# Optimization experiments

Hardware: AMD Instinct MI355X
Metric: run time of the kernel (lower is better)

The kernel has to match this reference:

```python
import jax, jax.numpy as jnp
import numpy as np

EPS = 1e-8  # torch CosineSimilarity default eps


def setup_inputs() -> dict:
    key = jax.random.key(0)
    k_emb, k_ei, k_w1, k_w2, k_b1, k_b2 = jax.random.split(key, 6)
    N, H, E = 50000, 256, 300000
    emb = jax.random.normal(k_emb, (N, H), dtype=jnp.float32)
    edge_index = jax.random.randint(k_ei, (2, E), 0, N, dtype=jnp.int64)
    # Xavier-uniform init for the two Linear layers (fan_in = fan_out = H)
    limit = float(np.sqrt(6.0 / (H + H)))
    W1 = jax.random.uniform(k_w1, (H, H), minval=-limit, maxval=limit, dtype=jnp.float32)
    W2 = jax.random.uniform(k_w2, (H, H), minval=-limit, maxval=limit, dtype=jnp.float32)
    b1 = jnp.zeros((H,), dtype=jnp.float32)
    b2 = jnp.zeros((H,), dtype=jnp.float32)
    return {"emb": emb, "edge_index": edge_index, "W1": W1, "b1": b1, "W2": W2, "b2": b2}


def _mlp(x, W1, b1, W2, b2):
    # Linear -> Dropout(eval: identity) -> ReLU -> Linear
    h = jax.nn.relu(x @ W1.T + b1)
    return h @ W2.T + b2


def _cosine(a, b):
    # torch.nn.CosineSimilarity(dim=1): dot / (max(||a||, eps) * max(||b||, eps))
    dot = jnp.sum(a * b, axis=1)
    na = jnp.maximum(jnp.linalg.norm(a, axis=1), EPS)
    nb = jnp.maximum(jnp.linalg.norm(b, axis=1), EPS)
    return dot / (na * nb)


def reference(emb, edge_index, W1, b1, W2, b2):
    col, row = edge_index[0], edge_index[1]
    f1 = emb[col]  # [E, H]
    f2 = emb[row]  # [E, H]
    g1 = _mlp(f1, W1, b1, W2, b2)
    g2 = _mlp(f2, W1, b1, W2, b2)
    return _cosine(g1, g2)  # [E] per-edge attention logits
```

## Files before the change

kernel.cpp:

```cpp
#include <hip/hip_runtime.h>
#include <stdint.h>

#define H 256
#define EPS 1e-8f

typedef __bf16 bf16x8 __attribute__((ext_vector_type(8)));
typedef float  f32x4  __attribute__((ext_vector_type(4)));

__device__ __forceinline__ unsigned short f2bf(float f) {
  unsigned u = __builtin_bit_cast(unsigned, f);
  u += 0x7FFFu + ((u >> 16) & 1u);
  return (unsigned short)(u >> 16);
}
__device__ __forceinline__ float bflo(unsigned u){ return __builtin_bit_cast(float, u << 16); }
__device__ __forceinline__ float bfhi(unsigned u){ return __builtin_bit_cast(float, u & 0xFFFF0000u); }

__device__ __forceinline__ void g2l16(const void* g, void* l) {
  __builtin_amdgcn_global_load_lds((__attribute__((address_space(1))) void*)g,
                                   (__attribute__((address_space(3))) void*)l, 16, 0, 0);
}

__global__ __launch_bounds__(256) void conv_bf16_kernel(
    const float* __restrict__ src, unsigned short* __restrict__ dst, int valid, int total) {
  int i = (blockIdx.x * 256 + threadIdx.x) * 4;
  if (i >= total) return;
  float4 v = make_float4(0.f, 0.f, 0.f, 0.f);
  if (i < valid) v = *(const float4*)(src + i);
  ushort4 o;
  o.x = f2bf(v.x); o.y = f2bf(v.y); o.z = f2bf(v.z); o.w = f2bf(v.w);
  *(ushort4*)(dst + i) = o;
}

template<bool RELU>
__global__ __launch_bounds__(256) void gemm_bt_kernel(
    const unsigned short* __restrict__ A,
    const unsigned short* __restrict__ B,
    const float* __restrict__ bias,
    unsigned short* __restrict__ C) {
  __shared__ unsigned short sA[128 * 32];
  __shared__ unsigned short sB[128 * 32];
  const int tid  = threadIdx.x;
  const int wave = tid >> 6, lane = tid & 63;
  const int quad = lane >> 4, l16 = lane & 15;
  const int wm = wave & 1, wn = wave >> 1;
  const size_t bm = blockIdx.x, bn = blockIdx.y;

  const int srow0 = (wave * 2 + 0) * 16 + (lane >> 2);
  const int srow1 = (wave * 2 + 1) * 16 + (lane >> 2);
  const int kch   = (lane & 3) * 8;
  const unsigned short* gA0 = A + ((bm * 128 + srow0) * H + kch);
  const unsigned short* gA1 = A + ((bm * 128 + srow1) * H + kch);
  const unsigned short* gB0 = B + ((bn * 128 + srow0) * H + kch);
  const unsigned short* gB1 = B + ((bn * 128 + srow1) * H + kch);
  unsigned short* lA0 = sA + (wave * 2 + 0) * 512 + lane * 8;
  unsigned short* lA1 = sA + (wave * 2 + 1) * 512 + lane * 8;
  unsigned short* lB0 = sB + (wave * 2 + 0) * 512 + lane * 8;
  unsigned short* lB1 = sB + (wave * 2 + 1) * 512 + lane * 8;

  f32x4 acc[4][4];
#pragma unroll
  for (int i = 0; i < 4; i++)
#pragma unroll
    for (int j = 0; j < 4; j++) acc[i][j] = (f32x4){0.f, 0.f, 0.f, 0.f};

#pragma unroll
  for (int kk = 0; kk < H / 32; ++kk) {
    const int k0 = kk * 32;
    if (kk) __syncthreads();
    g2l16(gA0 + k0, lA0);
    g2l16(gA1 + k0, lA1);
    g2l16(gB0 + k0, lB0);
    g2l16(gB1 + k0, lB1);
    __syncthreads();

    bf16x8 af[4], bfr[4];
#pragma unroll
    for (int i = 0; i < 4; i++)
      af[i] = *(const bf16x8*)(sA + ((wm * 64 + i * 16 + l16) * 32 + quad * 8));
#pragma unroll
    for (int j = 0; j < 4; j++)
      bfr[j] = *(const bf16x8*)(sB + ((wn * 64 + j * 16 + l16) * 32 + quad * 8));
#pragma unroll
    for (int i = 0; i < 4; i++)
#pragma unroll
      for (int j = 0; j < 4; j++)
        acc[i][j] = __builtin_amdgcn_mfma_f32_16x16x32_bf16(af[i], bfr[j], acc[i][j], 0, 0, 0);
  }

  const int row_base = (int)bm * 128 + wm * 64;
  const int col_base = (int)bn * 128 + wn * 64;
#pragma unroll
  for (int j = 0; j < 4; j++) {
    const int col = col_base + j * 16 + l16;
    const float bv = bias[col];
#pragma unroll
    for (int i = 0; i < 4; i++) {
#pragma unroll
      for (int r = 0; r < 4; r++) {
        const int row = row_base + i * 16 + quad * 4 + r;
        float v = acc[i][j][r] + bv;
        if (RELU) v = fmaxf(v, 0.f);
        C[(size_t)row * H + col] = f2bf(v);
      }
    }
  }
}

__global__ __launch_bounds__(256) void rownorm_kernel(
    const unsigned short* __restrict__ g, float* __restrict__ rn, int n) {
  int row = blockIdx.x * 4 + (threadIdx.x >> 6);
  if (row >= n) return;
  int lane = threadIdx.x & 63;
  uint2 a = ((const uint2*)(g + (size_t)row * H))[lane];
  float x0 = bflo(a.x), x1 = bfhi(a.x), x2 = bflo(a.y), x3 = bfhi(a.y);
  float ss = x0 * x0 + x1 * x1 + x2 * x2 + x3 * x3;
#pragma unroll
  for (int off = 32; off; off >>= 1) ss += __shfl_down(ss, off, 64);
  if (lane == 0) rn[row] = 1.f / fmaxf(sqrtf(ss), EPS);
}

__device__ __forceinline__ float dot_u4(uint4 a, uint4 b) {
  float s;
  s  = bflo(a.x) * bflo(b.x) + bfhi(a.x) * bfhi(b.x);
  s += bflo(a.y) * bflo(b.y) + bfhi(a.y) * bfhi(b.y);
  s += bflo(a.z) * bflo(b.z) + bfhi(a.z) * bfhi(b.z);
  s += bflo(a.w) * bflo(b.w) + bfhi(a.w) * bfhi(b.w);
  return s;
}

__global__ __launch_bounds__(256) void edge_cos_kernel(
    const int* __restrict__ ei, const unsigned short* __restrict__ g,
    const float* __restrict__ rn, float* __restrict__ out, int E) {
  const int lane = threadIdx.x & 63;
  const int wid  = threadIdx.x >> 6;
  const int l8   = lane & 7;
  const int sub  = lane >> 3;
  const int e    = blockIdx.x * 32 + wid * 8 + sub;
  if (e >= E) return;
  const int c = ei[e], r = ei[E + e];
  const uint4* gc = (const uint4*)(g + (size_t)c * H);
  const uint4* gr = (const uint4*)(g + (size_t)r * H);
  uint4 a0 = gc[l8], a1 = gc[l8 + 8], a2 = gc[l8 + 16], a3 = gc[l8 + 24];
  uint4 b0 = gr[l8], b1 = gr[l8 + 8], b2 = gr[l8 + 16], b3 = gr[l8 + 24];
  float d = dot_u4(a0, b0) + dot_u4(a1, b1) + dot_u4(a2, b2) + dot_u4(a3, b3);
  d += __shfl_xor(d, 4, 8);
  d += __shfl_xor(d, 2, 8);
  d += __shfl_xor(d, 1, 8);
  if (l8 == 0) out[e] = d * rn[c] * rn[r];
}

extern "C" void kernel_launch(void* const* d_in, const int* in_sizes, int n_in,
                              void* d_out, int out_size, void* d_ws, size_t ws_size,
                              hipStream_t stream) {
  const float* emb = (const float*)d_in[0];
  const int*   ei  = (const int*)d_in[1];
  const float* W1  = (const float*)d_in[2];
  const float* b1  = (const float*)d_in[3];
  const float* W2  = (const float*)d_in[4];
  const float* b2  = (const float*)d_in[5];
  float* out = (float*)d_out;

  const int NH = in_sizes[0];
  const int N  = NH / H;
  const int E  = in_sizes[1] / 2;
  const int Mp = ((N + 127) / 128) * 128;

  char* ws = (char*)d_ws;
  unsigned short* embB = (unsigned short*)ws; ws += (size_t)Mp * H * 2;
  unsigned short* hB   = (unsigned short*)ws; ws += (size_t)Mp * H * 2;
  unsigned short* gB   = (unsigned short*)ws; ws += (size_t)Mp * H * 2;
  unsigned short* w1B  = (unsigned short*)ws; ws += (size_t)H * H * 2;
  unsigned short* w2B  = (unsigned short*)ws; ws += (size_t)H * H * 2;
  float* rn            = (float*)ws;

  conv_bf16_kernel<<<(Mp * H / 4 + 255) / 256, 256, 0, stream>>>(emb, embB, NH, Mp * H);
  conv_bf16_kernel<<<(H * H / 4 + 255) / 256, 256, 0, stream>>>(W1, w1B, H * H, H * H);
  conv_bf16_kernel<<<(H * H / 4 + 255) / 256, 256, 0, stream>>>(W2, w2B, H * H, H * H);

  dim3 ggrid(Mp / 128, H / 128);
  gemm_bt_kernel<true ><<<ggrid, 256, 0, stream>>>(embB, w1B, b1, hB);
  gemm_bt_kernel<false><<<ggrid, 256, 0, stream>>>(hB, w2B, b2, gB);

  rownorm_kernel<<<(N + 3) / 4, 256, 0, stream>>>(gB, rn, N);
  edge_cos_kernel<<<(E + 31) / 32, 256, 0, stream>>>(ei, gB, rn, out, E);
}
```

Measured before the change: 182.2 us.

## Fuse both MLP GEMMs and row-norm into one kernel keeping hidden in LDS

Replaces the two separate GEMM launches and the rownorm kernel with a single kernel that processes 64 rows. It computes the first layer, keeps the ReLU hidden activations in a swizzled LDS buffer, runs the second layer from LDS, and computes the inverse row norms from the accumulators in registers. The two weight conversions are merged into one launch. This removes the global round trip for the hidden tensor, one reread of G, and several launches, at the cost of more LDS per block (lower occupancy) and full W1/W2 reloads per 64-row tile.

```diff
diff --git a/kernel.cpp b/kernel.cpp
--- a/kernel.cpp
+++ b/kernel.cpp
@@ -31,92 +31,185 @@
   *(ushort4*)(dst + i) = o;
 }
 
-template<bool RELU>
-__global__ __launch_bounds__(256) void gemm_bt_kernel(
+__global__ __launch_bounds__(256) void conv_w_kernel(
+    const float* __restrict__ W1, const float* __restrict__ W2,
+    unsigned short* __restrict__ w1B, unsigned short* __restrict__ w2B) {
+  int i = (blockIdx.x * 256 + threadIdx.x) * 4;
+  const int HH = H * H;
+  if (i >= 2 * HH) return;
+  const float* s = (i < HH) ? W1 : W2;
+  unsigned short* d = (i < HH) ? w1B : w2B;
+  int j = (i < HH) ? i : i - HH;
+  float4 v = *(const float4*)(s + j);
+  ushort4 o;
+  o.x = f2bf(v.x); o.y = f2bf(v.y); o.z = f2bf(v.z); o.w = f2bf(v.w);
+  *(ushort4*)(d + j) = o;
+}
+
+__global__ __launch_bounds__(256) void fused_mlp_kernel(
     const unsigned short* __restrict__ A,
-    const unsigned short* __restrict__ B,
-    const float* __restrict__ bias,
-    unsigned short* __restrict__ C) {
-  __shared__ unsigned short sA[128 * 32];
-  __shared__ unsigned short sB[128 * 32];
+    const unsigned short* __restrict__ W1,
+    const unsigned short* __restrict__ W2,
+    const float* __restrict__ b1, const float* __restrict__ b2,
+    unsigned short* __restrict__ G,
+    float* __restrict__ rn) {
+  __shared__ unsigned short sA[64 * 32];
+  __shared__ unsigned short sW[256 * 32];
+  __shared__ unsigned short sW2[256 * 32];
+  __shared__ unsigned short sH[64 * 256];
+  __shared__ float ssb[64][2];
+
   const int tid  = threadIdx.x;
   const int wave = tid >> 6, lane = tid & 63;
   const int quad = lane >> 4, l16 = lane & 15;
-  const int wm = wave & 1, wn = wave >> 1;
-  const size_t bm = blockIdx.x, bn = blockIdx.y;
-
-  const int srow0 = (wave * 2 + 0) * 16 + (lane >> 2);
-  const int srow1 = (wave * 2 + 1) * 16 + (lane >> 2);
-  const int kch   = (lane & 3) * 8;
-  const unsigned short* gA0 = A + ((bm * 128 + srow0) * H + kch);
-  const unsigned short* gA1 = A + ((bm * 128 + srow1) * H + kch);
-  const unsigned short* gB0 = B + ((bn * 128 + srow0) * H + kch);
-  const unsigned short* gB1 = B + ((bn * 128 + srow1) * H + kch);
-  unsigned short* lA0 = sA + (wave * 2 + 0) * 512 + lane * 8;
-  unsigned short* lA1 = sA + (wave * 2 + 1) * 512 + lane * 8;
-  unsigned short* lB0 = sB + (wave * 2 + 0) * 512 + lane * 8;
-  unsigned short* lB1 = sB + (wave * 2 + 1) * 512 + lane * 8;
-
-  f32x4 acc[4][4];
-#pragma unroll
-  for (int i = 0; i < 4; i++)
-#pragma unroll
-    for (int j = 0; j < 4; j++) acc[i][j] = (f32x4){0.f, 0.f, 0.f, 0.f};
-
-#pragma unroll
-  for (int kk = 0; kk < H / 32; ++kk) {
-    const int k0 = kk * 32;
-    if (kk) __syncthreads();
-    g2l16(gA0 + k0, lA0);
-    g2l16(gA1 + k0, lA1);
-    g2l16(gB0 + k0, lB0);
-    g2l16(gB1 + k0, lB1);
+  const int wr = wave >> 1, wn = wave & 1;
+  const size_t bm = blockIdx.x;
+
+  const int arow = tid >> 2, kch = (tid & 3) * 8;
+  const unsigned short* gA  = A  + ((bm * 64 + arow) * H + kch);
+  const unsigned short* gW1 = W1 + (size_t)arow * H + kch;
+  const unsigned short* gW2 = W2 + (size_t)arow * H + kch;
+  unsigned short* lA  = sA  + tid * 8;
+  unsigned short* lW  = sW  + tid * 8;
+  unsigned short* lW2 = sW2 + tid * 8;
+
+  f32x4 acc[8][2];
+#pragma unroll
+  for (int i = 0; i < 8; i++)
+#pragma unroll
+    for (int j = 0; j < 2; j++) acc[i][j] = (f32x4){0.f, 0.f, 0.f, 0.f};
+
+#pragma unroll
+  for (int ks = 0; ks < 8; ++ks) {
+    const int k0 = ks * 32;
+    if (ks) __syncthreads();
+    g2l16(gA + k0, lA);
+#pragma unroll
+    for (int c = 0; c < 4; c++)
+      g2l16(gW1 + (size_t)(c * 64) * H + k0, lW + c * 2048);
     __syncthreads();
 
-    bf16x8 af[4], bfr[4];
-#pragma unroll
-    for (int i = 0; i < 4; i++)
-      af[i] = *(const bf16x8*)(sA + ((wm * 64 + i * 16 + l16) * 32 + quad * 8));
-#pragma unroll
-    for (int j = 0; j < 4; j++)
-      bfr[j] = *(const bf16x8*)(sB + ((wn * 64 + j * 16 + l16) * 32 + quad * 8));
-#pragma unroll
-    for (int i = 0; i < 4; i++)
-#pragma unroll
-      for (int j = 0; j < 4; j++)
-        acc[i][j] = __builtin_amdgcn_mfma_f32_16x16x32_bf16(af[i], bfr[j], acc[i][j], 0, 0, 0);
-  }
-
-  const int row_base = (int)bm * 128 + wm * 64;
-  const int col_base = (int)bn * 128 + wn * 64;
-#pragma unroll
-  for (int j = 0; j < 4; j++) {
-    const int col = col_base + j * 16 + l16;
-    const float bv = bias[col];
-#pragma unroll
-    for (int i = 0; i < 4; i++) {
+    bf16x8 wf[8], af[2];
+#pragma unroll
+    for (int i = 0; i < 8; i++)
+      wf[i] = *(const bf16x8*)(sW + ((wn * 128 + i * 16 + l16) * 32 + quad * 8));
+#pragma unroll
+    for (int j = 0; j < 2; j++)
+      af[j] = *(const bf16x8*)(sA + ((wr * 32 + j * 16 + l16) * 32 + quad * 8));
+#pragma unroll
+    for (int i = 0; i < 8; i++)
+#pragma unroll
+      for (int j = 0; j < 2; j++)
+        acc[i][j] = __builtin_amdgcn_mfma_f32_16x16x32_bf16(wf[i], af[j], acc[i][j], 0, 0, 0);
+  }
+
+#pragma unroll
+  for (int c = 0; c < 4; c++)
+    g2l16(gW2 + (size_t)(c * 64) * H, lW2 + c * 2048);
+
+#pragma unroll
+  for (int i = 0; i < 8; i++) {
+    const int hcol = wn * 128 + i * 16 + quad * 4;
+    const float4 bv = *(const float4*)(b1 + hcol);
+#pragma unroll
+    for (int j = 0; j < 2; j++) {
+      const int row = wr * 32 + j * 16 + l16;
+      f32x4 v = acc[i][j];
+      unsigned short h0 = f2bf(fmaxf(v[0] + bv.x, 0.f));
+      unsigned short h1 = f2bf(fmaxf(v[1] + bv.y, 0.f));
+      unsigned short h2 = f2bf(fmaxf(v[2] + bv.z, 0.f));
+      unsigned short h3 = f2bf(fmaxf(v[3] + bv.w, 0.f));
+      uint2 p;
+      p.x = (unsigned)h0 | ((unsigned)h1 << 16);
+      p.y = (unsigned)h2 | ((unsigned)h3 << 16);
+      unsigned off = (unsigned)(row * 512 + hcol * 2) ^ ((unsigned)(row & 7) << 4);
+      *(uint2*)((char*)sH + off) = p;
+    }
+  }
+
+  __syncthreads();
+
+  f32x4 acc2[2][8];
+#pragma unroll
+  for (int i = 0; i < 2; i++)
+#pragma unroll
+    for (int j = 0; j < 8; j++) acc2[i][j] = (f32x4){0.f, 0.f, 0.f, 0.f};
+
+#pragma unroll
+  for (int ks = 0; ks < 8; ++ks) {
+    if (ks) {
+      __syncthreads();
+#pragma unroll
+      for (int c = 0; c < 4; c++)
+        g2l16(gW2 + (size_t)(c * 64) * H + ks * 32, lW2 + c * 2048);
+      __syncthreads();
+    }
+    bf16x8 hf[2], wf2[8];
+#pragma unroll
+    for (int i = 0; i < 2; i++) {
+      const int hrow = wr * 32 + i * 16 + l16;
+      unsigned off = (unsigned)(hrow * 512 + ks * 64 + quad * 16) ^ ((unsigned)(hrow & 7) << 4);
+      hf[i] = *(const bf16x8*)((const char*)sH + off);
+    }
+#pragma unroll
+    for (int j = 0; j < 8; j++)
+      wf2[j] = *(const bf16x8*)(sW2 + ((wn * 128 + j * 16 + l16) * 32 + quad * 8));
+#pragma unroll
+    for (int i = 0; i < 2; i++)
+#pragma unroll
+      for (int j = 0; j < 8; j++)
+        acc2[i][j] = __builtin_amdgcn_mfma_f32_16x16x32_bf16(hf[i], wf2[j], acc2[i][j], 0, 0, 0);
+  }
+
+  float b2v[8];
+#pragma unroll
+  for (int j = 0; j < 8; j++) b2v[j] = b2[wn * 128 + j * 16 + l16];
+#pragma unroll
+  for (int i = 0; i < 2; i++)
+#pragma unroll
+    for (int j = 0; j < 8; j++)
+#pragma unroll
+      for (int r = 0; r < 4; r++) acc2[i][j][r] += b2v[j];
+
+  float ss[2][4];
+#pragma unroll
+  for (int i = 0; i < 2; i++)
+#pragma unroll
+    for (int r = 0; r < 4; r++) {
+      float s = 0.f;
+#pragma unroll
+      for (int j = 0; j < 8; j++) s += acc2[i][j][r] * acc2[i][j][r];
+      ss[i][r] = s;
+    }
+#pragma unroll
+  for (int m = 1; m < 16; m <<= 1)
+#pragma unroll
+    for (int i = 0; i < 2; i++)
+#pragma unroll
+      for (int r = 0; r < 4; r++) ss[i][r] += __shfl_xor(ss[i][r], m, 64);
+  if (l16 == 0) {
+#pragma unroll
+    for (int i = 0; i < 2; i++)
+#pragma unroll
+      for (int r = 0; r < 4; r++) ssb[wr * 32 + i * 16 + quad * 4 + r][wn] = ss[i][r];
+  }
+  __syncthreads();
+  if (tid < 64) {
+    float s2 = ssb[tid][0] + ssb[tid][1];
+    rn[bm * 64 + tid] = 1.f / fmaxf(sqrtf(s2), EPS);
+  }
+
+#pragma unroll
+  for (int i = 0; i < 2; i++)
+#pragma unroll
+    for (int j = 0; j < 8; j++) {
+      const int gcol = wn * 128 + j * 16 + l16;
 #pragma unroll
       for (int r = 0; r < 4; r++) {
-        const int row = row_base + i * 16 + quad * 4 + r;
-        float v = acc[i][j][r] + bv;
-        if (RELU) v = fmaxf(v, 0.f);
-        C[(size_t)row * H + col] = f2bf(v);
+        const size_t grow = bm * 64 + wr * 32 + i * 16 + quad * 4 + r;
+        G[grow * H + gcol] = f2bf(acc2[i][j][r]);
       }
     }
-  }
-}
-
-__global__ __launch_bounds__(256) void rownorm_kernel(
-    const unsigned short* __restrict__ g, float* __restrict__ rn, int n) {
-  int row = blockIdx.x * 4 + (threadIdx.x >> 6);
-  if (row >= n) return;
-  int lane = threadIdx.x & 63;
-  uint2 a = ((const uint2*)(g + (size_t)row * H))[lane];
-  float x0 = bflo(a.x), x1 = bfhi(a.x), x2 = bflo(a.y), x3 = bfhi(a.y);
-  float ss = x0 * x0 + x1 * x1 + x2 * x2 + x3 * x3;
-#pragma unroll
-  for (int off = 32; off; off >>= 1) ss += __shfl_down(ss, off, 64);
-  if (lane == 0) rn[row] = 1.f / fmaxf(sqrtf(ss), EPS);
 }
 
 __device__ __forceinline__ float dot_u4(uint4 a, uint4 b) {
@@ -163,24 +256,19 @@
   const int NH = in_sizes[0];
   const int N  = NH / H;
   const int E  = in_sizes[1] / 2;
-  const int Mp = ((N + 127) / 128) * 128;
+  const int Mp = ((N + 63) / 64) * 64;
 
   char* ws = (char*)d_ws;
   unsigned short* embB = (unsigned short*)ws; ws += (size_t)Mp * H * 2;
-  unsigned short* hB   = (unsigned short*)ws; ws += (size_t)Mp * H * 2;
   unsigned short* gB   = (unsigned short*)ws; ws += (size_t)Mp * H * 2;
   unsigned short* w1B  = (unsigned short*)ws; ws += (size_t)H * H * 2;
   unsigned short* w2B  = (unsigned short*)ws; ws += (size_t)H * H * 2;
   float* rn            = (float*)ws;
 
   conv_bf16_kernel<<<(Mp * H / 4 + 255) / 256, 256, 0, stream>>>(emb, embB, NH, Mp * H);
-  conv_bf16_kernel<<<(H * H / 4 + 255) / 256, 256, 0, stream>>>(W1, w1B, H * H, H * H);
-  conv_bf16_kernel<<<(H * H / 4 + 255) / 256, 256, 0, stream>>>(W2, w2B, H * H, H * H);
-
-  dim3 ggrid(Mp / 128, H / 128);
-  gemm_bt_kernel<true ><<<ggrid, 256, 0, stream>>>(embB, w1B, b1, hB);
-  gemm_bt_kernel<false><<<ggrid, 256, 0, stream>>>(hB, w2B, b2, gB);
-
-  rownorm_kernel<<<(N + 3) / 4, 256, 0, stream>>>(gB, rn, N);
+  conv_w_kernel<<<(2 * H * H / 4 + 255) / 256, 256, 0, stream>>>(W1, W2, w1B, w2B);
+
+  fused_mlp_kernel<<<Mp / 64, 256, 0, stream>>>(embB, w1B, w2B, b1, b2, gB, rn);
+
   edge_cos_kernel<<<(E + 31) / 32, 256, 0, stream>>>(ei, gB, rn, out, E);
 }
```

Result: faster. 165.7 us (-9.1%).

## Fuse bf16 conversion, norms into persistent GEMM kernels with LDS-resident weights

Applied to the files above, without the earlier changes.

Replaces the separate conversion kernels, two tiled GEMMs and the rownorm kernel with a persistent 256-block GEMM that converts the full 256x256 weight matrix to bf16 once into 128KB of LDS. Each block loops over 128-row tiles with register-prefetched, double-buffered A tiles in swizzled LDS. The first GEMM reads fp32 emb directly and converts on the fly. The second GEMM computes row sum-of-squares in its epilogue to produce inverse norms. This removes several launches and the intermediate bf16 embedding round-trip, but the large LDS footprint limits occupancy to one block per CU.

```diff
diff --git a/kernel.cpp b/kernel.cpp
--- a/kernel.cpp
+++ b/kernel.cpp
@@ -15,108 +15,158 @@
 __device__ __forceinline__ float bflo(unsigned u){ return __builtin_bit_cast(float, u << 16); }
 __device__ __forceinline__ float bfhi(unsigned u){ return __builtin_bit_cast(float, u & 0xFFFF0000u); }
 
-__device__ __forceinline__ void g2l16(const void* g, void* l) {
-  __builtin_amdgcn_global_load_lds((__attribute__((address_space(1))) void*)g,
-                                   (__attribute__((address_space(3))) void*)l, 16, 0, 0);
-}
-
-__global__ __launch_bounds__(256) void conv_bf16_kernel(
-    const float* __restrict__ src, unsigned short* __restrict__ dst, int valid, int total) {
-  int i = (blockIdx.x * 256 + threadIdx.x) * 4;
-  if (i >= total) return;
-  float4 v = make_float4(0.f, 0.f, 0.f, 0.f);
-  if (i < valid) v = *(const float4*)(src + i);
-  ushort4 o;
-  o.x = f2bf(v.x); o.y = f2bf(v.y); o.z = f2bf(v.z); o.w = f2bf(v.w);
-  *(ushort4*)(dst + i) = o;
-}
-
-template<bool RELU>
-__global__ __launch_bounds__(256) void gemm_bt_kernel(
-    const unsigned short* __restrict__ A,
-    const unsigned short* __restrict__ B,
-    const float* __restrict__ bias,
-    unsigned short* __restrict__ C) {
-  __shared__ unsigned short sA[128 * 32];
-  __shared__ unsigned short sB[128 * 32];
+__device__ __forceinline__ uint4 pack8(float4 a, float4 b) {
+  uint4 p;
+  p.x = (unsigned)f2bf(a.x) | ((unsigned)f2bf(a.y) << 16);
+  p.y = (unsigned)f2bf(a.z) | ((unsigned)f2bf(a.w) << 16);
+  p.z = (unsigned)f2bf(b.x) | ((unsigned)f2bf(b.y) << 16);
+  p.w = (unsigned)f2bf(b.z) | ((unsigned)f2bf(b.w) << 16);
+  return p;
+}
+
+#define SW_BYTES   131072
+#define SA_BYTES   8192
+#define LDS_BYTES  (SW_BYTES + 2 * SA_BYTES + 1024)
+#define SA(b) (lds + SW_BYTES + (b) * SA_BYTES)
+
+template<bool FIRST>
+__global__ __launch_bounds__(512) void mlp_gemm_kernel(
+    const void* __restrict__ Asrc, const float* __restrict__ Wf,
+    const float* __restrict__ bias, unsigned short* __restrict__ Out,
+    float* __restrict__ rn, int N, int ntiles) {
+  extern __shared__ char lds[];
+  char* sW = lds;
+  float* ssb = (float*)(lds + SW_BYTES + 2 * SA_BYTES);
+
   const int tid  = threadIdx.x;
   const int wave = tid >> 6, lane = tid & 63;
   const int quad = lane >> 4, l16 = lane & 15;
-  const int wm = wave & 1, wn = wave >> 1;
-  const size_t bm = blockIdx.x, bn = blockIdx.y;
-
-  const int srow0 = (wave * 2 + 0) * 16 + (lane >> 2);
-  const int srow1 = (wave * 2 + 1) * 16 + (lane >> 2);
-  const int kch   = (lane & 3) * 8;
-  const unsigned short* gA0 = A + ((bm * 128 + srow0) * H + kch);
-  const unsigned short* gA1 = A + ((bm * 128 + srow1) * H + kch);
-  const unsigned short* gB0 = B + ((bn * 128 + srow0) * H + kch);
-  const unsigned short* gB1 = B + ((bn * 128 + srow1) * H + kch);
-  unsigned short* lA0 = sA + (wave * 2 + 0) * 512 + lane * 8;
-  unsigned short* lA1 = sA + (wave * 2 + 1) * 512 + lane * 8;
-  unsigned short* lB0 = sB + (wave * 2 + 0) * 512 + lane * 8;
-  unsigned short* lB1 = sB + (wave * 2 + 1) * 512 + lane * 8;
-
-  f32x4 acc[4][4];
-#pragma unroll
-  for (int i = 0; i < 4; i++)
-#pragma unroll
-    for (int j = 0; j < 4; j++) acc[i][j] = (f32x4){0.f, 0.f, 0.f, 0.f};
-
-#pragma unroll
-  for (int kk = 0; kk < H / 32; ++kk) {
-    const int k0 = kk * 32;
-    if (kk) __syncthreads();
-    g2l16(gA0 + k0, lA0);
-    g2l16(gA1 + k0, lA1);
-    g2l16(gB0 + k0, lB0);
-    g2l16(gB1 + k0, lB1);
-    __syncthreads();
-
-    bf16x8 af[4], bfr[4];
-#pragma unroll
-    for (int i = 0; i < 4; i++)
-      af[i] = *(const bf16x8*)(sA + ((wm * 64 + i * 16 + l16) * 32 + quad * 8));
-#pragma unroll
-    for (int j = 0; j < 4; j++)
-      bfr[j] = *(const bf16x8*)(sB + ((wn * 64 + j * 16 + l16) * 32 + quad * 8));
-#pragma unroll
-    for (int i = 0; i < 4; i++)
-#pragma unroll
-      for (int j = 0; j < 4; j++)
-        acc[i][j] = __builtin_amdgcn_mfma_f32_16x16x32_bf16(af[i], bfr[j], acc[i][j], 0, 0, 0);
+  const int wr = wave >> 1, wn = wave & 1;
+
+#pragma unroll 4
+  for (int it = 0; it < 32; ++it) {
+    int g = it * 512 + tid;
+    int row = g >> 5;
+    const float* src = Wf + (size_t)row * H + (g & 31) * 8;
+    float4 w0 = *(const float4*)(src);
+    float4 w1 = *(const float4*)(src + 4);
+    uint4 p = pack8(w0, w1);
+    unsigned off = ((unsigned)g * 16u) ^ (((unsigned)row & 7u) << 4);
+    *(uint4*)(sW + off) = p;
   }
 
-  const int row_base = (int)bm * 128 + wm * 64;
-  const int col_base = (int)bn * 128 + wn * 64;
-#pragma unroll
-  for (int j = 0; j < 4; j++) {
-    const int col = col_base + j * 16 + l16;
-    const float bv = bias[col];
-#pragma unroll
-    for (int i = 0; i < 4; i++) {
-#pragma unroll
-      for (int r = 0; r < 4; r++) {
-        const int row = row_base + i * 16 + quad * 4 + r;
-        float v = acc[i][j][r] + bv;
-        if (RELU) v = fmaxf(v, 0.f);
-        C[(size_t)row * H + col] = f2bf(v);
-      }
-    }
+  const int arow = tid >> 2, ac = tid & 3;
+  const unsigned aoff = ((unsigned)tid * 16u) ^ ((((unsigned)tid >> 3) & 3u) << 4);
+  const float4 z4 = make_float4(0.f, 0.f, 0.f, 0.f);
+
+  for (int t = blockIdx.x; t < ntiles; t += gridDim.x) {
+    const int r0 = t * 128 + arow;
+    const float* gA_f = nullptr; const unsigned short* gA_h = nullptr;
+    bool avalid = true;
+    if constexpr (FIRST) {
+      avalid = r0 < N;
+      gA_f = (const float*)Asrc + (size_t)(avalid ? r0 : N - 1) * H + ac * 8;
+    } else {
+      gA_h = (const unsigned short*)Asrc + (size_t)r0 * H + ac * 8;
+    }
+
+    float4 rf[3][2]; uint4 rh[3];
+#define LOADA(kt, s)                                                            \
+    do {                                                                        \
+      if constexpr (FIRST) {                                                    \
+        rf[s][0] = *(const float4*)(gA_f + (kt) * 32);                          \
+        rf[s][1] = *(const float4*)(gA_f + (kt) * 32 + 4);                      \
+      } else {                                                                  \
+        rh[s] = *(const uint4*)(gA_h + (kt) * 32);                              \
+      }                                                                         \
+    } while (0)
+#define WRITEA(s, bufp)                                                         \
+    do {                                                                        \
+      uint4 p;                                                                  \
+      if constexpr (FIRST) {                                                    \
+        float4 t0 = avalid ? rf[s][0] : z4;                                     \
+        float4 t1 = avalid ? rf[s][1] : z4;                                     \
+        p = pack8(t0, t1);                                                      \
+      } else { p = rh[s]; }                                                     \
+      *(uint4*)((bufp) + aoff) = p;                                             \
+    } while (0)
+
+    LOADA(0, 0); LOADA(1, 1); LOADA(2, 2);
+    WRITEA(0, SA(0));
+
+    f32x4 acc[8][2];
+#pragma unroll
+    for (int i = 0; i < 8; i++)
+#pragma unroll
+      for (int j = 0; j < 2; j++) acc[i][j] = (f32x4){0.f, 0.f, 0.f, 0.f};
+
+#pragma unroll
+    for (int kt = 0; kt < 8; ++kt) {
+      asm volatile("s_waitcnt lgkmcnt(0)" ::: "memory");
+      __builtin_amdgcn_s_barrier();
+      if (kt < 5) LOADA(kt + 3, kt % 3);
+      if (kt < 7) WRITEA((kt + 1) % 3, SA((kt + 1) & 1));
+
+      bf16x8 wf[8], af0, af1;
+#pragma unroll
+      for (int i = 0; i < 8; i++) {
+        unsigned wrow = (unsigned)(wn * 128 + i * 16 + l16);
+        unsigned woff = (wrow * 512u + (unsigned)kt * 64u + (unsigned)quad * 16u)
+                        ^ ((wrow & 7u) << 4);
+        wf[i] = *(const bf16x8*)(sW + woff);
+      }
+      {
+        unsigned ar0 = (unsigned)(wr * 32 + l16), ar1 = ar0 + 16;
+        const char* ab = SA(kt & 1);
+        af0 = *(const bf16x8*)(ab + ((ar0 * 64u + (unsigned)quad * 16u) ^ (((ar0 >> 1) & 3u) << 4)));
+        af1 = *(const bf16x8*)(ab + ((ar1 * 64u + (unsigned)quad * 16u) ^ (((ar1 >> 1) & 3u) << 4)));
+      }
+#pragma unroll
+      for (int i = 0; i < 8; i++) {
+        acc[i][0] = __builtin_amdgcn_mfma_f32_16x16x32_bf16(wf[i], af0, acc[i][0], 0, 0, 0);
+        acc[i][1] = __builtin_amdgcn_mfma_f32_16x16x32_bf16(wf[i], af1, acc[i][1], 0, 0, 0);
+      }
+    }
+
+    float ss0 = 0.f, ss1 = 0.f;
+#pragma unroll
+    for (int i = 0; i < 8; i++) {
+      const int col0 = wn * 128 + i * 16 + quad * 4;
+      const float4 bv = *(const float4*)(bias + col0);
+#pragma unroll
+      for (int j = 0; j < 2; j++) {
+        const int row = t * 128 + wr * 32 + j * 16 + l16;
+        f32x4 v = acc[i][j];
+        float v0 = v[0] + bv.x, v1 = v[1] + bv.y, v2 = v[2] + bv.z, v3 = v[3] + bv.w;
+        if constexpr (FIRST) {
+          v0 = fmaxf(v0, 0.f); v1 = fmaxf(v1, 0.f);
+          v2 = fmaxf(v2, 0.f); v3 = fmaxf(v3, 0.f);
+        } else {
+          float s = v0 * v0 + v1 * v1 + v2 * v2 + v3 * v3;
+          if (j == 0) ss0 += s; else ss1 += s;
+        }
+        uint2 p;
+        p.x = (unsigned)f2bf(v0) | ((unsigned)f2bf(v1) << 16);
+        p.y = (unsigned)f2bf(v2) | ((unsigned)f2bf(v3) << 16);
+        *(uint2*)(Out + (size_t)row * H + col0) = p;
+      }
+    }
+    if constexpr (!FIRST) {
+      ss0 += __shfl_xor(ss0, 16, 64); ss0 += __shfl_xor(ss0, 32, 64);
+      ss1 += __shfl_xor(ss1, 16, 64); ss1 += __shfl_xor(ss1, 32, 64);
+      if (quad == 0) {
+        ssb[(wr * 32 + l16) * 2 + wn]      = ss0;
+        ssb[(wr * 32 + 16 + l16) * 2 + wn] = ss1;
+      }
+      __syncthreads();
+      if (tid < 128) {
+        float s2 = ssb[tid * 2 + 0] + ssb[tid * 2 + 1];
+        rn[t * 128 + tid] = 1.f / fmaxf(sqrtf(s2), EPS);
+      }
+    }
+#undef LOADA
+#undef WRITEA
   }
-}
-
-__global__ __launch_bounds__(256) void rownorm_kernel(
-    const unsigned short* __restrict__ g, float* __restrict__ rn, int n) {
-  int row = blockIdx.x * 4 + (threadIdx.x >> 6);
-  if (row >= n) return;
-  int lane = threadIdx.x & 63;
-  uint2 a = ((const uint2*)(g + (size_t)row * H))[lane];
-  float x0 = bflo(a.x), x1 = bfhi(a.x), x2 = bflo(a.y), x3 = bfhi(a.y);
-  float ss = x0 * x0 + x1 * x1 + x2 * x2 + x3 * x3;
-#pragma unroll
-  for (int off = 32; off; off >>= 1) ss += __shfl_down(ss, off, 64);
-  if (lane == 0) rn[row] = 1.f / fmaxf(sqrtf(ss), EPS);
 }
 
 __device__ __forceinline__ float dot_u4(uint4 a, uint4 b) {
@@ -164,23 +214,23 @@
   const int N  = NH / H;
   const int E  = in_sizes[1] / 2;
   const int Mp = ((N + 127) / 128) * 128;
+  const int ntiles = Mp / 128;
 
   char* ws = (char*)d_ws;
-  unsigned short* embB = (unsigned short*)ws; ws += (size_t)Mp * H * 2;
-  unsigned short* hB   = (unsigned short*)ws; ws += (size_t)Mp * H * 2;
-  unsigned short* gB   = (unsigned short*)ws; ws += (size_t)Mp * H * 2;
-  unsigned short* w1B  = (unsigned short*)ws; ws += (size_t)H * H * 2;
-  unsigned short* w2B  = (unsigned short*)ws; ws += (size_t)H * H * 2;
-  float* rn            = (float*)ws;
-
-  conv_bf16_kernel<<<(Mp * H / 4 + 255) / 256, 256, 0, stream>>>(emb, embB, NH, Mp * H);
-  conv_bf16_kernel<<<(H * H / 4 + 255) / 256, 256, 0, stream>>>(W1, w1B, H * H, H * H);
-  conv_bf16_kernel<<<(H * H / 4 + 255) / 256, 256, 0, stream>>>(W2, w2B, H * H, H * H);
-
-  dim3 ggrid(Mp / 128, H / 128);
-  gemm_bt_kernel<true ><<<ggrid, 256, 0, stream>>>(embB, w1B, b1, hB);
-  gemm_bt_kernel<false><<<ggrid, 256, 0, stream>>>(hB, w2B, b2, gB);
-
-  rownorm_kernel<<<(N + 3) / 4, 256, 0, stream>>>(gB, rn, N);
+  unsigned short* hB = (unsigned short*)ws; ws += (size_t)Mp * H * 2;
+  unsigned short* gB = (unsigned short*)ws; ws += (size_t)Mp * H * 2;
+  float* rn          = (float*)ws;
+
+  static bool attr_set = false;
+  if (!attr_set) {
+    hipFuncSetAttribute(reinterpret_cast<const void*>(mlp_gemm_kernel<true>),
+                        hipFuncAttributeMaxDynamicSharedMemorySize, LDS_BYTES);
+    hipFuncSetAttribute(reinterpret_cast<const void*>(mlp_gemm_kernel<false>),
+                        hipFuncAttributeMaxDynamicSharedMemorySize, LDS_BYTES);
+    attr_set = true;
+  }
+
+  mlp_gemm_kernel<true ><<<256, 512, LDS_BYTES, stream>>>(emb, W1, b1, hB, nullptr, N, ntiles);
+  mlp_gemm_kernel<false><<<256, 512, LDS_BYTES, stream>>>(hB,  W2, b2, gB, rn,      N, ntiles);
   edge_cos_kernel<<<(E + 31) / 32, 256, 0, stream>>>(ei, gB, rn, out, E);
 }
```

New measurement: 192.2 us. +5.5%, slower.
